# Performance work log

Measured on AMD Instinct MI355X. Metric: run time of the kernel, lower is better.

Reference implementation:

```python
import jax, jax.numpy as jnp
import numpy as np

L, N, E, D_MODEL, H = 3, 50000, 600000, 128, 8
D = D_MODEL // H          # per-head dim = 16
DFF = 4 * D_MODEL         # feedforward hidden = 512


def prelu(x, a):
    return jnp.where(x >= 0, x, a * x)


def layernorm(x, scale, bias, eps=1e-5):
    m = x.mean(-1, keepdims=True)
    v = x.var(-1, keepdims=True)
    return (x - m) * jax.lax.rsqrt(v + eps) * scale + bias


def setup_inputs() -> dict:
    key = jax.random.key(0)
    ks = jax.random.split(key, 16)
    s = 1.0 / np.sqrt(D_MODEL)
    return {
        "in_feats": jax.random.normal(ks[0], (N, D_MODEL), jnp.float32),
        "src": jax.random.randint(ks[1], (E,), 0, N, jnp.int32),
        "dst": jax.random.randint(ks[2], (E,), 0, N, jnp.int32),
        # per-layer stacked parameters
        "W": jax.random.normal(ks[3], (L, D_MODEL, D_MODEL), jnp.float32) * s,
        "attn_l": jax.random.normal(ks[4], (L, H, D), jnp.float32) * s,
        "attn_r": jax.random.normal(ks[5], (L, H, D), jnp.float32) * s,
        "conv_bias": jnp.zeros((L, H, D), jnp.float32),
        "a_conv": jnp.full((L,), 0.25, jnp.float32),   # PReLU slope after conv
        "ln_scale": jnp.ones((L, D_MODEL), jnp.float32),
        "ln_bias": jnp.zeros((L, D_MODEL), jnp.float32),
        "W1": jax.random.normal(ks[6], (L, D_MODEL, DFF), jnp.float32) * s,
        "b1": jnp.zeros((L, DFF), jnp.float32),
        "W2": jax.random.normal(ks[7], (L, DFF, D_MODEL), jnp.float32) / np.sqrt(DFF),
        "b2": jnp.zeros((L, D_MODEL), jnp.float32),
        "a_ff": jnp.full((L,), 0.25, jnp.float32),     # PReLU slope in FF
    }


def _gat_conv(x, src, dst, W, attn_l, attn_r, conv_bias, a_conv):
    # DGL GATConv: project, per-edge additive attention, edge-softmax over dst, scatter.
    z = (x @ W).reshape(N, H, D)                    # [N,H,D]
    el = (z * attn_l).sum(-1)                       # [N,H]
    er = (z * attn_r).sum(-1)                       # [N,H]
    e = jax.nn.leaky_relu(el[src] + er[dst], 0.2)   # [E,H]
    emax = jax.ops.segment_max(e, dst, num_segments=N)
    emax = jnp.where(jnp.isfinite(emax), emax, 0.0)  # zero in-degree guard
    ex = jnp.exp(e - emax[dst])                     # [E,H]
    denom = jax.ops.segment_sum(ex, dst, num_segments=N)  # [N,H]
    msg = ex[:, :, None] * z[src]                   # [E,H,D]
    agg = jax.ops.segment_sum(msg, dst, num_segments=N)   # [N,H,D]
    out = agg / jnp.maximum(denom, 1e-9)[:, :, None]
    out = prelu(out + conv_bias, a_conv)            # bias + PReLU activation
    return out.reshape(N, H * D)


def reference(in_feats, src, dst, W, attn_l, attn_r, conv_bias, a_conv,
              ln_scale, ln_bias, W1, b1, W2, b2, a_ff):
    outputs = []
    x = in_feats
    for l in range(L):
        h = _gat_conv(x, src, dst, W[l], attn_l[l], attn_r[l], conv_bias[l], a_conv[l])
        h = layernorm(h, ln_scale[l], ln_bias[l])   # layer['norm']
        # FeedForward, norm_first=True, sharing the same LayerNorm params
        hn = layernorm(h, ln_scale[l], ln_bias[l])
        ff = prelu(hn @ W1[l] + b1[l], a_ff[l]) @ W2[l] + b2[l]
        x = h + ff
        outputs.append(x)
    return jnp.stack(outputs)                       # [L, N, d]
```

## Files before the change

### kernel.cpp

```cpp
#include <hip/hip_runtime.h>

#define DM 128
#define NH 8
#define DFF 512

typedef __attribute__((ext_vector_type(8))) short bf16x8;
typedef __attribute__((ext_vector_type(4))) float f32x4;

#define WAITVM(N) do { asm volatile("s_waitcnt vmcnt(" #N ")" ::: "memory"); \
                       __builtin_amdgcn_sched_barrier(0); } while (0)
#define WAITLGKM0 do { asm volatile("s_waitcnt lgkmcnt(0)" ::: "memory"); \
                       __builtin_amdgcn_sched_barrier(0); } while (0)

__device__ __forceinline__ short f2bf(float f) {
    union { float f; unsigned u; } v; v.f = f;
    unsigned r = v.u + 0x7fffu + ((v.u >> 16) & 1u);
    return (short)(r >> 16);
}
__device__ __forceinline__ float bf2f(unsigned short b) {
    union { unsigned u; float f; } v; v.u = ((unsigned)b) << 16; return v.f;
}

template<int ROWS, int NT>
__device__ __forceinline__ void stage_tile(
    const short* __restrict__ g, int row0, int maxrow, int rstride, int kbase,
    short* s, int tid)
{
    const int lane = tid & 63;
#pragma unroll
    for (int rr = 0; rr < ROWS * 16 / NT; ++rr) {
        int idx = rr * NT + tid;
        int row = idx >> 4, kc = idx & 15;
        int rg = row0 + row;
        rg = (rg < maxrow) ? rg : (maxrow - 1);
        const short* src = g + (size_t)rg * rstride + kbase
                         + ((kc ^ (row & 15)) << 3);
        short* dst = s + (size_t)(idx - lane) * 8;
        __builtin_amdgcn_global_load_lds(
            (const __attribute__((address_space(1))) void*)src,
            (__attribute__((address_space(3))) void*)dst, 16, 0, 0);
    }
}

__device__ __forceinline__ bf16x8 frag_ld(const short* s, int row, int ks, int g)
{
    return *(const bf16x8*)(s + row * 128 + ((((ks << 2) + g) ^ (row & 15)) << 3));
}

template<bool PRELU, int NOUT>
__global__ __launch_bounds__(512, 4) void gemm_k128_stream(
    const short* __restrict__ A, const short* __restrict__ Bt,
    const float* __restrict__ bias, const float* __restrict__ affp,
    int M, short* __restrict__ outbf)
{
    __shared__ __align__(16) short sW[128 * 128];
    __shared__ __align__(16) short sA[3][64 * 128];

    const int tid = threadIdx.x;
    const int wave = tid >> 6, lane = tid & 63;
    const int wm = wave >> 2, wn = wave & 3;
    const int bn = blockIdx.x * 128;
    const int fr = lane & 15, g = lane >> 4;
    const int lr4 = g << 2;
    const int nT = (M + 63) >> 6;
    const int GY = gridDim.y;
    const int t0 = blockIdx.y;
    const int nLoc = (t0 < nT) ? ((nT - 1 - t0) / GY + 1) : 0;

    float bb[2]; float aff = 0.0f;
    if constexpr (PRELU) {
        aff = *affp;
#pragma unroll
        for (int cg = 0; cg < 2; ++cg)
            bb[cg] = bias[bn + wn * 32 + cg * 16 + fr];
    }

    stage_tile<128, 512>(Bt + (size_t)bn * 128, 0, 128, 128, 0, sW, tid);
    if (nLoc > 0) stage_tile<64, 512>(A, t0 * 64, M, 128, 0, sA[0], tid);
    if (nLoc > 1) stage_tile<64, 512>(A, (t0 + GY) * 64, M, 128, 0, sA[1], tid);

    for (int i = 0; i < nLoc; ++i) {
        const int t = t0 + i * GY;
        if (i >= 1 && i + 1 < nLoc)
            stage_tile<64, 512>(A, (t + GY) * 64, M, 128, 0, sA[(i + 1) % 3], tid);

        if (i == 0) { if (nLoc > 1) { WAITVM(2); } else { WAITVM(0); } }
        else if (i + 1 < nLoc) { WAITVM(18); }
        else { WAITVM(16); }
        __builtin_amdgcn_s_barrier();

        const short* sAb = sA[i % 3];
        f32x4 acc[2][2];
#pragma unroll
        for (int ii = 0; ii < 2; ++ii)
#pragma unroll
            for (int cg = 0; cg < 2; ++cg) acc[ii][cg] = (f32x4)0.0f;

#pragma unroll
        for (int ks = 0; ks < 4; ++ks) {
            bf16x8 af[2], bf[2];
#pragma unroll
            for (int ii = 0; ii < 2; ++ii)
                af[ii] = frag_ld(sAb, wm * 32 + ii * 16 + fr, ks, g);
#pragma unroll
            for (int cg = 0; cg < 2; ++cg)
                bf[cg] = frag_ld(sW, wn * 32 + cg * 16 + fr, ks, g);
#pragma unroll
            for (int ii = 0; ii < 2; ++ii)
#pragma unroll
                for (int cg = 0; cg < 2; ++cg)
                    acc[ii][cg] = __builtin_amdgcn_mfma_f32_16x16x32_bf16(
                        af[ii], bf[cg], acc[ii][cg], 0, 0, 0);
        }

#pragma unroll
        for (int ii = 0; ii < 2; ++ii)
#pragma unroll
            for (int cg = 0; cg < 2; ++cg) {
                int colL = wn * 32 + cg * 16 + fr;
#pragma unroll
                for (int r = 0; r < 4; ++r) {
                    int row = t * 64 + wm * 32 + ii * 16 + lr4 + r;
                    if (row < M) {
                        float v = acc[ii][cg][r];
                        if constexpr (PRELU) {
                            v += bb[cg];
                            v = (v >= 0.0f) ? v : aff * v;
                        }
                        outbf[(size_t)row * NOUT + bn + colL] = f2bf(v);
                    }
                }
            }
    }
}

__global__ __launch_bounds__(512, 2) void ffn2z(
    const short* __restrict__ H1, const short* __restrict__ W2t,
    const short* __restrict__ h_bf, const float* __restrict__ b2,
    const short* __restrict__ Wnt, int has_next, int M,
    float* __restrict__ xo, short* __restrict__ z_next)
{
    __shared__ __align__(16) short sWn[128 * 128];
    __shared__ __align__(16) short sA[2][64 * 128];
    __shared__ __align__(16) short sB[2][128 * 128];

    const int tid = threadIdx.x;
    const int wave = tid >> 6, lane = tid & 63;
    const int wm = wave >> 2, wn = wave & 3;
    const int bm = blockIdx.x * 64;
    const int fr = lane & 15, g = lane >> 4;
    const int lr4 = g << 2;

    f32x4 acc[2][2];
#pragma unroll
    for (int ii = 0; ii < 2; ++ii)
#pragma unroll
        for (int cg = 0; cg < 2; ++cg) acc[ii][cg] = (f32x4)0.0f;

    stage_tile<128, 512>(Wnt, 0, 128, DM, 0, sWn, tid);
    stage_tile<64, 512>(H1, bm, M, DFF, 0, sA[0], tid);
    stage_tile<128, 512>(W2t, 0, 128, DFF, 0, sB[0], tid);

#pragma unroll
    for (int c = 0; c < 4; ++c) {
        __builtin_amdgcn_s_barrier();
        if (c < 3) {
            stage_tile<64, 512>(H1, bm, M, DFF, (c + 1) * 128, sA[(c + 1) & 1], tid);
            stage_tile<128, 512>(W2t, 0, 128, DFF, (c + 1) * 128, sB[(c + 1) & 1], tid);
            WAITVM(6);
        } else {
            WAITVM(0);
        }
        __builtin_amdgcn_s_barrier();

        const short* a = sA[c & 1];
        const short* b = sB[c & 1];
#pragma unroll
        for (int ks = 0; ks < 4; ++ks) {
            bf16x8 af[2], bf[2];
#pragma unroll
            for (int ii = 0; ii < 2; ++ii)
                af[ii] = frag_ld(a, wm * 32 + ii * 16 + fr, ks, g);
#pragma unroll
            for (int cg = 0; cg < 2; ++cg)
                bf[cg] = frag_ld(b, wn * 32 + cg * 16 + fr, ks, g);
#pragma unroll
            for (int ii = 0; ii < 2; ++ii)
#pragma unroll
                for (int cg = 0; cg < 2; ++cg)
                    acc[ii][cg] = __builtin_amdgcn_mfma_f32_16x16x32_bf16(
                        af[ii], bf[cg], acc[ii][cg], 0, 0, 0);
        }
    }

    short* sX = sA[0];
#pragma unroll
    for (int ii = 0; ii < 2; ++ii)
#pragma unroll
        for (int cg = 0; cg < 2; ++cg) {
            int colL = wn * 32 + cg * 16 + fr;
            float bbv = b2[colL];
#pragma unroll
            for (int r = 0; r < 4; ++r) {
                int rowL = wm * 32 + ii * 16 + lr4 + r;
                int row = bm + rowL;
                int rc = (row < M) ? row : (M - 1);
                float v = acc[ii][cg][r] + bbv
                        + bf2f((unsigned short)h_bf[(size_t)rc * DM + colL]);
                if (row < M) xo[(size_t)row * DM + colL] = v;
                if (has_next) {
                    int kc = colL >> 3;
                    sX[rowL * 128 + ((kc ^ (rowL & 15)) << 3) + (colL & 7)]
                        = f2bf(v);
                }
            }
        }
    if (!has_next) return;

    WAITLGKM0;
    __builtin_amdgcn_s_barrier();

    f32x4 acc3[2][2];
#pragma unroll
    for (int ii = 0; ii < 2; ++ii)
#pragma unroll
        for (int cg = 0; cg < 2; ++cg) acc3[ii][cg] = (f32x4)0.0f;

#pragma unroll
    for (int ks = 0; ks < 4; ++ks) {
        bf16x8 af[2], bf[2];
#pragma unroll
        for (int ii = 0; ii < 2; ++ii)
            af[ii] = frag_ld(sX, wm * 32 + ii * 16 + fr, ks, g);
#pragma unroll
        for (int cg = 0; cg < 2; ++cg)
            bf[cg] = frag_ld(sWn, wn * 32 + cg * 16 + fr, ks, g);
#pragma unroll
        for (int ii = 0; ii < 2; ++ii)
#pragma unroll
            for (int cg = 0; cg < 2; ++cg)
                acc3[ii][cg] = __builtin_amdgcn_mfma_f32_16x16x32_bf16(
                    af[ii], bf[cg], acc3[ii][cg], 0, 0, 0);
    }
#pragma unroll
    for (int ii = 0; ii < 2; ++ii)
#pragma unroll
        for (int cg = 0; cg < 2; ++cg) {
            int colL = wn * 32 + cg * 16 + fr;
#pragma unroll
            for (int r = 0; r < 4; ++r) {
                int row = bm + wm * 32 + ii * 16 + lr4 + r;
                if (row < M)
                    z_next[(size_t)row * DM + colL] = f2bf(acc3[ii][cg][r]);
            }
        }
}

__global__ void conv_all_kernel(
    const float* __restrict__ W, const float* __restrict__ W1,
    const float* __restrict__ W2, const float* __restrict__ xin,
    short* __restrict__ Wt, short* __restrict__ W1t, short* __restrict__ W2t,
    short* __restrict__ xbf, int nFeat, int nL)
{
    int idx = blockIdx.x * blockDim.x + threadIdx.x;
    const int n0 = nL * DM * DM, n1 = nL * DM * DFF, n2 = nL * DFF * DM;
    if (idx < n0) {
        int l = idx / (DM * DM), rem = idx & (DM * DM - 1);
        int r = rem >> 7, c = rem & 127;
        Wt[(size_t)l * DM * DM + c * DM + r] = f2bf(W[idx]);
        return;
    }
    idx -= n0;
    if (idx < n1) {
        int l = idx / (DM * DFF), rem = idx & (DM * DFF - 1);
        int r = rem >> 9, c = rem & 511;
        W1t[(size_t)l * DM * DFF + (size_t)c * DM + r] = f2bf(W1[idx]);
        return;
    }
    idx -= n1;
    if (idx < n2) {
        int l = idx / (DFF * DM), rem = idx & (DFF * DM - 1);
        int r = rem >> 7, c = rem & 127;
        W2t[(size_t)l * DFF * DM + (size_t)c * DFF + r] = f2bf(W2[idx]);
        return;
    }
    idx -= n2;
    if (idx < nFeat) xbf[idx] = f2bf(xin[idx]);
}

__global__ void el_er_kernel(const short* __restrict__ z,
                             const float* __restrict__ al,
                             const float* __restrict__ ar,
                             float* __restrict__ el, float* __restrict__ er, int N)
{
    int idx = blockIdx.x * blockDim.x + threadIdx.x;
    if (idx >= N * NH) return;
    int n = idx >> 3, h = idx & 7;
    const unsigned* zp = (const unsigned*)(z + (size_t)n * DM + h * 16);
    const float* alp = al + h * 16;
    const float* arp = ar + h * 16;
    float sl = 0.0f, sr = 0.0f;
#pragma unroll
    for (int d2 = 0; d2 < 8; ++d2) {
        unsigned u = zp[d2];
        float z0 = bf2f((unsigned short)(u & 0xffff));
        float z1 = bf2f((unsigned short)(u >> 16));
        sl = fmaf(z0, alp[2 * d2], sl);     sl = fmaf(z1, alp[2 * d2 + 1], sl);
        sr = fmaf(z0, arp[2 * d2], sr);     sr = fmaf(z1, arp[2 * d2 + 1], sr);
    }
    el[idx] = sl;
    er[idx] = sr;
}

__global__ void hist_kernel(const int* __restrict__ dst, int* __restrict__ deg, int E)
{
    int e = blockIdx.x * blockDim.x + threadIdx.x;
    if (e < E) atomicAdd(&deg[dst[e]], 1);
}

__global__ void scan1_kernel(const int* __restrict__ deg, int* __restrict__ incl,
                             int* __restrict__ bsum, int N)
{
    __shared__ int sm[256];
    int i = blockIdx.x * 256 + threadIdx.x;
    int v = (i < N) ? deg[i] : 0;
    sm[threadIdx.x] = v;
    __syncthreads();
    for (int off = 1; off < 256; off <<= 1) {
        int t = (threadIdx.x >= off) ? sm[threadIdx.x - off] : 0;
        __syncthreads();
        sm[threadIdx.x] += t;
        __syncthreads();
    }
    if (i < N) incl[i] = sm[threadIdx.x];
    if (threadIdx.x == 255) bsum[blockIdx.x] = sm[255];
}

__global__ void scan2_kernel(int* __restrict__ bsum, int nb)
{
    __shared__ int sm[256];
    int v = (threadIdx.x < nb) ? bsum[threadIdx.x] : 0;
    sm[threadIdx.x] = v;
    __syncthreads();
    for (int off = 1; off < 256; off <<= 1) {
        int t = (threadIdx.x >= off) ? sm[threadIdx.x - off] : 0;
        __syncthreads();
        sm[threadIdx.x] += t;
        __syncthreads();
    }
    if (threadIdx.x < nb) bsum[threadIdx.x] = sm[threadIdx.x];
}

__global__ void scan3_kernel(const int* __restrict__ incl, const int* __restrict__ bsum,
                             int* __restrict__ row_ptr, int N)
{
    int i = blockIdx.x * 256 + threadIdx.x;
    if (i < N) {
        int off = (blockIdx.x > 0) ? bsum[blockIdx.x - 1] : 0;
        row_ptr[i + 1] = incl[i] + off;
    }
    if (i == 0) row_ptr[0] = 0;
}

__global__ void scatter_kernel(const int* __restrict__ src, const int* __restrict__ dst,
                               const int* __restrict__ row_ptr, int* __restrict__ cursor,
                               int* __restrict__ csr_src, int E)
{
    int e = blockIdx.x * blockDim.x + threadIdx.x;
    if (e >= E) return;
    int t = dst[e];
    int pos = atomicAdd(&cursor[t], 1);
    csr_src[row_ptr[t] + pos] = src[e];
}

__global__ __launch_bounds__(256) void gat_agg_ln_kernel(
    const int* __restrict__ row_ptr, const int* __restrict__ csr_src,
    const short* __restrict__ z, const float* __restrict__ el,
    const float* __restrict__ er, const float* __restrict__ cb,
    const float* __restrict__ a_conv,
    const float* __restrict__ scale, const float* __restrict__ bias,
    short* __restrict__ h_out, short* __restrict__ hn_out, int N)
{
    int wave = threadIdx.x >> 6, lane = threadIdx.x & 63;
    int t = blockIdx.x * 4 + wave;
    if (t >= N) return;
    int h = lane >> 3;
    int c0 = 2 * lane, c1 = c0 + 1;
    float er_t = er[t * NH + h];
    int e0 = row_ptr[t], e1 = row_ptr[t + 1];
    float acc0 = 0.0f, acc1 = 0.0f, den = 0.0f;
    const unsigned* zw = (const unsigned*)z;

    int e = e0;
    int s[8];
    bool have = (e + 8 <= e1);
    if (have) {
#pragma unroll
        for (int k = 0; k < 8; ++k) s[k] = csr_src[e + k];
    }
    while (have) {
        float x[8]; unsigned u[8];
#pragma unroll
        for (int k = 0; k < 8; ++k) x[k] = el[s[k] * NH + h];
#pragma unroll
        for (int k = 0; k < 8; ++k) u[k] = zw[(size_t)s[k] * 64 + lane];
        int en = e + 8;
        bool hv2 = (en + 8 <= e1);
        int sn[8];
#pragma unroll
        for (int k = 0; k < 8; ++k) sn[k] = hv2 ? csr_src[en + k] : 0;
#pragma unroll
        for (int k = 0; k < 8; ++k) {
            float v = x[k] + er_t;
            v = (v >= 0.0f) ? v : 0.2f * v;
            float w = __expf(v);
            den += w;
            acc0 = fmaf(w, bf2f((unsigned short)(u[k] & 0xffff)), acc0);
            acc1 = fmaf(w, bf2f((unsigned short)(u[k] >> 16)),   acc1);
        }
#pragma unroll
        for (int k = 0; k < 8; ++k) s[k] = sn[k];
        e = en; have = hv2;
    }
    for (; e + 4 <= e1; e += 4) {
        int s4[4];
#pragma unroll
        for (int k = 0; k < 4; ++k) s4[k] = csr_src[e + k];
        float x[4]; unsigned u[4];
#pragma unroll
        for (int k = 0; k < 4; ++k) x[k] = el[s4[k] * NH + h];
#pragma unroll
        for (int k = 0; k < 4; ++k) u[k] = zw[(size_t)s4[k] * 64 + lane];
#pragma unroll
        for (int k = 0; k < 4; ++k) {
            float v = x[k] + er_t;
            v = (v >= 0.0f) ? v : 0.2f * v;
            float w = __expf(v);
            den += w;
            acc0 = fmaf(w, bf2f((unsigned short)(u[k] & 0xffff)), acc0);
            acc1 = fmaf(w, bf2f((unsigned short)(u[k] >> 16)),   acc1);
        }
    }
    for (; e < e1; ++e) {
        int sv = csr_src[e];
        float v = el[sv * NH + h] + er_t;
        v = (v >= 0.0f) ? v : 0.2f * v;
        float w = __expf(v);
        den += w;
        unsigned u = zw[(size_t)sv * 64 + lane];
        acc0 = fmaf(w, bf2f((unsigned short)(u & 0xffff)), acc0);
        acc1 = fmaf(w, bf2f((unsigned short)(u >> 16)), acc1);
    }

    float a = *a_conv;
    float inv = 1.0f / fmaxf(den, 1e-9f);
    float o0 = acc0 * inv + cb[c0];
    float o1 = acc1 * inv + cb[c1];
    o0 = (o0 >= 0.0f) ? o0 : a * o0;
    o1 = (o1 >= 0.0f) ? o1 : a * o1;

    float sc0 = scale[c0], sc1 = scale[c1];
    float bi0 = bias[c0], bi1 = bias[c1];

    float s1 = o0 + o1, ss = o0 * o0 + o1 * o1;
#pragma unroll
    for (int off = 32; off > 0; off >>= 1) {
        s1 += __shfl_xor(s1, off, 64);
        ss += __shfl_xor(ss, off, 64);
    }
    float mean = s1 * (1.0f / 128.0f);
    float var = ss * (1.0f / 128.0f) - mean * mean;
    float rstd = rsqrtf(var + 1e-5f);
    float h0 = (o0 - mean) * rstd * sc0 + bi0;
    float h1 = (o1 - mean) * rstd * sc1 + bi1;
    unsigned hlo = (unsigned short)f2bf(h0);
    unsigned hhi = (unsigned short)f2bf(h1);
    ((unsigned*)h_out)[(size_t)t * 64 + lane] = hlo | (hhi << 16);

    s1 = h0 + h1; ss = h0 * h0 + h1 * h1;
#pragma unroll
    for (int off = 32; off > 0; off >>= 1) {
        s1 += __shfl_xor(s1, off, 64);
        ss += __shfl_xor(ss, off, 64);
    }
    mean = s1 * (1.0f / 128.0f);
    var = ss * (1.0f / 128.0f) - mean * mean;
    rstd = rsqrtf(var + 1e-5f);
    unsigned lo = (unsigned short)f2bf((h0 - mean) * rstd * sc0 + bi0);
    unsigned hi = (unsigned short)f2bf((h1 - mean) * rstd * sc1 + bi1);
    ((unsigned*)hn_out)[(size_t)t * 64 + lane] = lo | (hi << 16);
}

extern "C" void kernel_launch(void* const* d_in, const int* in_sizes, int n_in,
                              void* d_out, int out_size, void* d_ws, size_t ws_size,
                              hipStream_t stream)
{
    const float* in_feats = (const float*)d_in[0];
    const int*   src      = (const int*)d_in[1];
    const int*   dst      = (const int*)d_in[2];
    const float* W        = (const float*)d_in[3];
    const float* attn_l   = (const float*)d_in[4];
    const float* attn_r   = (const float*)d_in[5];
    const float* convb    = (const float*)d_in[6];
    const float* a_conv   = (const float*)d_in[7];
    const float* ln_scale = (const float*)d_in[8];
    const float* ln_bias  = (const float*)d_in[9];
    const float* W1       = (const float*)d_in[10];
    const float* b1       = (const float*)d_in[11];
    const float* W2       = (const float*)d_in[12];
    const float* b2       = (const float*)d_in[13];
    const float* a_ff     = (const float*)d_in[14];
    float* out = (float*)d_out;

    const int N = in_sizes[0] / DM;
    const int E = in_sizes[1];
    const int L = in_sizes[7];

    char* wsb = (char*)d_ws;
    size_t off = 0;
    auto alloc = [&](size_t bytes) { char* p = wsb + off; off += (bytes + 255) & ~(size_t)255; return p; };

    short* z_bf  = (short*)alloc((size_t)N * DM * sizeof(short));
    short* h_bf  = (short*)alloc((size_t)N * DM * sizeof(short));
    short* hn_bf = (short*)alloc((size_t)N * DM * sizeof(short));
    short* x_bf  = (short*)alloc((size_t)N * DM * sizeof(short));
    short* H1    = (short*)alloc((size_t)N * DFF * sizeof(short));
    float* el    = (float*)alloc((size_t)N * NH * sizeof(float));
    float* er    = (float*)alloc((size_t)N * NH * sizeof(float));
    short* Wt    = (short*)alloc((size_t)L * DM * DM * sizeof(short));
    short* W1t   = (short*)alloc((size_t)L * DFF * DM * sizeof(short));
    short* W2t   = (short*)alloc((size_t)L * DM * DFF * sizeof(short));
    int* deg     = (int*)alloc((size_t)N * sizeof(int));
    int* incl    = (int*)alloc((size_t)N * sizeof(int));
    int* bsum    = (int*)alloc(256 * sizeof(int));
    int* row_ptr = (int*)alloc((size_t)(N + 1) * sizeof(int));
    int* cursor  = (int*)alloc((size_t)N * sizeof(int));
    int* csr_src = (int*)alloc((size_t)E * sizeof(int));

    const int gM64  = (N + 63) / 64;
    const int nbScan = (N + 255) / 256;

    hipMemsetAsync(deg, 0, (size_t)N * sizeof(int), stream);
    hipMemsetAsync(cursor, 0, (size_t)N * sizeof(int), stream);
    hist_kernel<<<(E + 255) / 256, 256, 0, stream>>>(dst, deg, E);
    scan1_kernel<<<nbScan, 256, 0, stream>>>(deg, incl, bsum, N);
    scan2_kernel<<<1, 256, 0, stream>>>(bsum, nbScan);
    scan3_kernel<<<nbScan, 256, 0, stream>>>(incl, bsum, row_ptr, N);
    scatter_kernel<<<(E + 255) / 256, 256, 0, stream>>>(src, dst, row_ptr, cursor, csr_src, E);

    {
        int total = L * DM * DM + L * DM * DFF + L * DFF * DM + N * DM;
        conv_all_kernel<<<(total + 255) / 256, 256, 0, stream>>>(
            W, W1, W2, in_feats, Wt, W1t, W2t, x_bf, N * DM, L);
    }

    gemm_k128_stream<false, DM><<<dim3(1, 512), 512, 0, stream>>>(
        x_bf, Wt, nullptr, nullptr, N, z_bf);
    el_er_kernel<<<(N * NH + 255) / 256, 256, 0, stream>>>(
        z_bf, attn_l, attn_r, el, er, N);

    for (int l = 0; l < L; ++l) {
        float* xo = out + (size_t)l * N * DM;
        const int has_next = (l + 1 < L) ? 1 : 0;
        const short* Wnt = has_next ? (Wt + (size_t)(l + 1) * DM * DM) : Wt;

        gat_agg_ln_kernel<<<(N + 3) / 4, 256, 0, stream>>>(
            row_ptr, csr_src, z_bf, el, er, convb + (size_t)l * DM, a_conv + l,
            ln_scale + (size_t)l * DM, ln_bias + (size_t)l * DM, h_bf, hn_bf, N);

        gemm_k128_stream<true, DFF><<<dim3(4, 128), 512, 0, stream>>>(
            hn_bf, W1t + (size_t)l * DFF * DM, b1 + (size_t)l * DFF, a_ff + l, N, H1);

        ffn2z<<<gM64, 512, 0, stream>>>(
            H1, W2t + (size_t)l * DM * DFF, h_bf, b2 + (size_t)l * DM,
            Wnt, has_next, N, xo, z_bf);

        if (has_next)
            el_er_kernel<<<(N * NH + 255) / 256, 256, 0, stream>>>(
                z_bf, attn_l + (size_t)(l + 1) * NH * 16,
                attn_r + (size_t)(l + 1) * NH * 16, el, er, N);
    }
}
```

Measured before the change: 504.0 us.

## Fuse FFN up-projection into FFN2 kernel and halve-wave GAT aggregation

Merges the W1 GEMM (with bias and PReLU) into the FFN2 plus next-layer projection kernel. The 64x512 hidden activation now stays in LDS instead of round-tripping through global memory, and the W1, W2 and Wn weight tiles stream through a shared double buffer. Separately, the GAT aggregation kernel now maps one destination node to half a wave with 4 channels per lane, using 8-byte gathers. The fusion removes a kernel launch and the H1 traffic, at the cost of larger LDS use (sH is 64KB), which may lower occupancy, and a longer serial chain of barriers.

```diff
diff --git a/kernel.cpp b/kernel.cpp
--- a/kernel.cpp
+++ b/kernel.cpp
@@ -6,6 +6,7 @@
 
 typedef __attribute__((ext_vector_type(8))) short bf16x8;
 typedef __attribute__((ext_vector_type(4))) float f32x4;
+typedef __attribute__((ext_vector_type(2))) unsigned uintx2;
 
 #define WAITVM(N) do { asm volatile("s_waitcnt vmcnt(" #N ")" ::: "memory"); \
                        __builtin_amdgcn_sched_barrier(0); } while (0)
@@ -45,6 +46,13 @@
 __device__ __forceinline__ bf16x8 frag_ld(const short* s, int row, int ks, int g)
 {
     return *(const bf16x8*)(s + row * 128 + ((((ks << 2) + g) ^ (row & 15)) << 3));
+}
+
+__device__ __forceinline__ bf16x8 frag_ld_h(const short* s, int row, int c,
+                                            int ks, int g)
+{
+    int ch = ((ks << 2) + g) ^ (row & 15);
+    return *(const bf16x8*)(s + row * 512 + c * 128 + (ch << 3));
 }
 
 template<bool PRELU, int NOUT>
@@ -134,126 +142,172 @@
     }
 }
 
-__global__ __launch_bounds__(512, 2) void ffn2z(
-    const short* __restrict__ H1, const short* __restrict__ W2t,
-    const short* __restrict__ h_bf, const float* __restrict__ b2,
-    const short* __restrict__ Wnt, int has_next, int M,
-    float* __restrict__ xo, short* __restrict__ z_next)
-{
-    __shared__ __align__(16) short sWn[128 * 128];
-    __shared__ __align__(16) short sA[2][64 * 128];
-    __shared__ __align__(16) short sB[2][128 * 128];
+__global__ __launch_bounds__(512, 2) void ffn12z(
+    const short* __restrict__ hn, const short* __restrict__ W1t,
+    const short* __restrict__ W2t, const short* __restrict__ h_bf,
+    const float* __restrict__ b1, const float* __restrict__ b2,
+    const float* __restrict__ affp, const short* __restrict__ Wnt,
+    int has_next, int M, float* __restrict__ xo, short* __restrict__ z_next)
+{
+    __shared__ __align__(16) short sH[64 * 512];
+    __shared__ __align__(16) short sW[2][128 * 128];
 
     const int tid = threadIdx.x;
     const int wave = tid >> 6, lane = tid & 63;
     const int wm = wave >> 2, wn = wave & 3;
     const int bm = blockIdx.x * 64;
     const int fr = lane & 15, g = lane >> 4;
-    const int lr4 = g << 2;
-
-    f32x4 acc[2][2];
+    const int lr4 = g << 2, fk8 = g << 3;
+
+    stage_tile<128, 512>(W1t, 0, 512, 128, 0, sW[0], tid);
+
+    bf16x8 ah[2][4];
+#pragma unroll
+    for (int ii = 0; ii < 2; ++ii) {
+        int row = bm + wm * 32 + ii * 16 + fr;
+        row = (row < M) ? row : (M - 1);
+#pragma unroll
+        for (int ks = 0; ks < 4; ++ks)
+            ah[ii][ks] = *(const bf16x8*)(hn + (size_t)row * DM + ks * 32 + fk8);
+    }
+    float aff = *affp;
+
+    f32x4 acc2[2][2];
 #pragma unroll
     for (int ii = 0; ii < 2; ++ii)
 #pragma unroll
-        for (int cg = 0; cg < 2; ++cg) acc[ii][cg] = (f32x4)0.0f;
-
-    stage_tile<128, 512>(Wnt, 0, 128, DM, 0, sWn, tid);
-    stage_tile<64, 512>(H1, bm, M, DFF, 0, sA[0], tid);
-    stage_tile<128, 512>(W2t, 0, 128, DFF, 0, sB[0], tid);
-
-#pragma unroll
-    for (int c = 0; c < 4; ++c) {
-        __builtin_amdgcn_s_barrier();
-        if (c < 3) {
-            stage_tile<64, 512>(H1, bm, M, DFF, (c + 1) * 128, sA[(c + 1) & 1], tid);
-            stage_tile<128, 512>(W2t, 0, 128, DFF, (c + 1) * 128, sB[(c + 1) & 1], tid);
-            WAITVM(6);
+        for (int cg = 0; cg < 2; ++cg) acc2[ii][cg] = (f32x4)0.0f;
+
+#pragma unroll
+    for (int j = 0; j < 9; ++j) {
+        if (j >= 1) { WAITLGKM0; __builtin_amdgcn_s_barrier(); }
+        if (j + 1 < 9) {
+            int jj = j + 1;
+            if (jj < 4)
+                stage_tile<128, 512>(W1t, jj * 128, 512, 128, 0, sW[jj & 1], tid);
+            else if (jj < 8)
+                stage_tile<128, 512>(W2t, 0, 128, 512, (jj - 4) * 128, sW[jj & 1], tid);
+            else
+                stage_tile<128, 512>(Wnt, 0, 128, 128, 0, sW[jj & 1], tid);
+            WAITVM(4);
         } else {
             WAITVM(0);
         }
         __builtin_amdgcn_s_barrier();
 
-        const short* a = sA[c & 1];
-        const short* b = sB[c & 1];
-#pragma unroll
-        for (int ks = 0; ks < 4; ++ks) {
-            bf16x8 af[2], bf[2];
+        if (j < 4) {
+            f32x4 a1[2][2];
 #pragma unroll
             for (int ii = 0; ii < 2; ++ii)
-                af[ii] = frag_ld(a, wm * 32 + ii * 16 + fr, ks, g);
-#pragma unroll
-            for (int cg = 0; cg < 2; ++cg)
-                bf[cg] = frag_ld(b, wn * 32 + cg * 16 + fr, ks, g);
+#pragma unroll
+                for (int cg = 0; cg < 2; ++cg) a1[ii][cg] = (f32x4)0.0f;
+#pragma unroll
+            for (int ks = 0; ks < 4; ++ks) {
+                bf16x8 bf[2];
+#pragma unroll
+                for (int cg = 0; cg < 2; ++cg)
+                    bf[cg] = frag_ld(sW[j & 1], wn * 32 + cg * 16 + fr, ks, g);
+#pragma unroll
+                for (int ii = 0; ii < 2; ++ii)
+#pragma unroll
+                    for (int cg = 0; cg < 2; ++cg)
+                        a1[ii][cg] = __builtin_amdgcn_mfma_f32_16x16x32_bf16(
+                            ah[ii][ks], bf[cg], a1[ii][cg], 0, 0, 0);
+            }
 #pragma unroll
             for (int ii = 0; ii < 2; ++ii)
 #pragma unroll
+                for (int cg = 0; cg < 2; ++cg) {
+                    int colC = wn * 32 + cg * 16 + fr;
+                    float bb = b1[j * 128 + colC];
+#pragma unroll
+                    for (int r = 0; r < 4; ++r) {
+                        int rowL = wm * 32 + ii * 16 + lr4 + r;
+                        float v = a1[ii][cg][r] + bb;
+                        v = (v >= 0.0f) ? v : aff * v;
+                        int ch = (colC >> 3) ^ (rowL & 15);
+                        sH[rowL * 512 + j * 128 + (ch << 3) + (colC & 7)] = f2bf(v);
+                    }
+                }
+        } else if (j < 8) {
+            int c = j - 4;
+#pragma unroll
+            for (int ks = 0; ks < 4; ++ks) {
+                bf16x8 af[2], bf[2];
+#pragma unroll
+                for (int ii = 0; ii < 2; ++ii)
+                    af[ii] = frag_ld_h(sH, wm * 32 + ii * 16 + fr, c, ks, g);
+#pragma unroll
                 for (int cg = 0; cg < 2; ++cg)
-                    acc[ii][cg] = __builtin_amdgcn_mfma_f32_16x16x32_bf16(
-                        af[ii], bf[cg], acc[ii][cg], 0, 0, 0);
-        }
-    }
-
-    short* sX = sA[0];
-#pragma unroll
-    for (int ii = 0; ii < 2; ++ii)
-#pragma unroll
-        for (int cg = 0; cg < 2; ++cg) {
-            int colL = wn * 32 + cg * 16 + fr;
-            float bbv = b2[colL];
-#pragma unroll
-            for (int r = 0; r < 4; ++r) {
-                int rowL = wm * 32 + ii * 16 + lr4 + r;
-                int row = bm + rowL;
-                int rc = (row < M) ? row : (M - 1);
-                float v = acc[ii][cg][r] + bbv
-                        + bf2f((unsigned short)h_bf[(size_t)rc * DM + colL]);
-                if (row < M) xo[(size_t)row * DM + colL] = v;
-                if (has_next) {
-                    int kc = colL >> 3;
-                    sX[rowL * 128 + ((kc ^ (rowL & 15)) << 3) + (colL & 7)]
-                        = f2bf(v);
+                    bf[cg] = frag_ld(sW[j & 1], wn * 32 + cg * 16 + fr, ks, g);
+#pragma unroll
+                for (int ii = 0; ii < 2; ++ii)
+#pragma unroll
+                    for (int cg = 0; cg < 2; ++cg)
+                        acc2[ii][cg] = __builtin_amdgcn_mfma_f32_16x16x32_bf16(
+                            af[ii], bf[cg], acc2[ii][cg], 0, 0, 0);
+            }
+        } else {
+#pragma unroll
+            for (int ii = 0; ii < 2; ++ii)
+#pragma unroll
+                for (int cg = 0; cg < 2; ++cg) {
+                    int colL = wn * 32 + cg * 16 + fr;
+                    float bbv = b2[colL];
+#pragma unroll
+                    for (int r = 0; r < 4; ++r) {
+                        int rowL = wm * 32 + ii * 16 + lr4 + r;
+                        int row = bm + rowL;
+                        int rc = (row < M) ? row : (M - 1);
+                        float v = acc2[ii][cg][r] + bbv
+                                + bf2f((unsigned short)h_bf[(size_t)rc * DM + colL]);
+                        if (row < M) xo[(size_t)row * DM + colL] = v;
+                        if (has_next) {
+                            int kc = colL >> 3;
+                            sH[rowL * 128 + ((kc ^ (rowL & 15)) << 3) + (colL & 7)]
+                                = f2bf(v);
+                        }
+                    }
                 }
+            if (has_next) {
+                WAITLGKM0;
+                __builtin_amdgcn_s_barrier();
+                f32x4 a3[2][2];
+#pragma unroll
+                for (int ii = 0; ii < 2; ++ii)
+#pragma unroll
+                    for (int cg = 0; cg < 2; ++cg) a3[ii][cg] = (f32x4)0.0f;
+#pragma unroll
+                for (int ks = 0; ks < 4; ++ks) {
+                    bf16x8 af[2], bf[2];
+#pragma unroll
+                    for (int ii = 0; ii < 2; ++ii)
+                        af[ii] = frag_ld(sH, wm * 32 + ii * 16 + fr, ks, g);
+#pragma unroll
+                    for (int cg = 0; cg < 2; ++cg)
+                        bf[cg] = frag_ld(sW[0], wn * 32 + cg * 16 + fr, ks, g);
+#pragma unroll
+                    for (int ii = 0; ii < 2; ++ii)
+#pragma unroll
+                        for (int cg = 0; cg < 2; ++cg)
+                            a3[ii][cg] = __builtin_amdgcn_mfma_f32_16x16x32_bf16(
+                                af[ii], bf[cg], a3[ii][cg], 0, 0, 0);
+                }
+#pragma unroll
+                for (int ii = 0; ii < 2; ++ii)
+#pragma unroll
+                    for (int cg = 0; cg < 2; ++cg) {
+                        int colL = wn * 32 + cg * 16 + fr;
+#pragma unroll
+                        for (int r = 0; r < 4; ++r) {
+                            int row = bm + wm * 32 + ii * 16 + lr4 + r;
+                            if (row < M)
+                                z_next[(size_t)row * DM + colL] = f2bf(a3[ii][cg][r]);
+                        }
+                    }
             }
         }
-    if (!has_next) return;
-
-    WAITLGKM0;
-    __builtin_amdgcn_s_barrier();
-
-    f32x4 acc3[2][2];
-#pragma unroll
-    for (int ii = 0; ii < 2; ++ii)
-#pragma unroll
-        for (int cg = 0; cg < 2; ++cg) acc3[ii][cg] = (f32x4)0.0f;
-
-#pragma unroll
-    for (int ks = 0; ks < 4; ++ks) {
-        bf16x8 af[2], bf[2];
-#pragma unroll
-        for (int ii = 0; ii < 2; ++ii)
-            af[ii] = frag_ld(sX, wm * 32 + ii * 16 + fr, ks, g);
-#pragma unroll
-        for (int cg = 0; cg < 2; ++cg)
-            bf[cg] = frag_ld(sWn, wn * 32 + cg * 16 + fr, ks, g);
-#pragma unroll
-        for (int ii = 0; ii < 2; ++ii)
-#pragma unroll
-            for (int cg = 0; cg < 2; ++cg)
-                acc3[ii][cg] = __builtin_amdgcn_mfma_f32_16x16x32_bf16(
-                    af[ii], bf[cg], acc3[ii][cg], 0, 0, 0);
-    }
-#pragma unroll
-    for (int ii = 0; ii < 2; ++ii)
-#pragma unroll
-        for (int cg = 0; cg < 2; ++cg) {
-            int colL = wn * 32 + cg * 16 + fr;
-#pragma unroll
-            for (int r = 0; r < 4; ++r) {
-                int row = bm + wm * 32 + ii * 16 + lr4 + r;
-                if (row < M)
-                    z_next[(size_t)row * DM + colL] = f2bf(acc3[ii][cg][r]);
-            }
-        }
+    }
 }
 
 __global__ void conv_all_kernel(
@@ -382,14 +436,14 @@
     short* __restrict__ h_out, short* __restrict__ hn_out, int N)
 {
     int wave = threadIdx.x >> 6, lane = threadIdx.x & 63;
-    int t = blockIdx.x * 4 + wave;
+    int half = lane >> 5, l32 = lane & 31;
+    int t = blockIdx.x * 8 + wave * 2 + half;
     if (t >= N) return;
-    int h = lane >> 3;
-    int c0 = 2 * lane, c1 = c0 + 1;
+    int h = l32 >> 2;
+    int cbase = l32 * 4;
     float er_t = er[t * NH + h];
     int e0 = row_ptr[t], e1 = row_ptr[t + 1];
-    float acc0 = 0.0f, acc1 = 0.0f, den = 0.0f;
-    const unsigned* zw = (const unsigned*)z;
+    float a0 = 0.0f, a1 = 0.0f, a2 = 0.0f, a3 = 0.0f, den = 0.0f;
 
     int e = e0;
     int s[8];
@@ -399,11 +453,12 @@
         for (int k = 0; k < 8; ++k) s[k] = csr_src[e + k];
     }
     while (have) {
-        float x[8]; unsigned u[8];
+        float x[8]; uintx2 u[8];
 #pragma unroll
         for (int k = 0; k < 8; ++k) x[k] = el[s[k] * NH + h];
 #pragma unroll
-        for (int k = 0; k < 8; ++k) u[k] = zw[(size_t)s[k] * 64 + lane];
+        for (int k = 0; k < 8; ++k)
+            u[k] = *(const uintx2*)(z + (size_t)s[k] * DM + cbase);
         int en = e + 8;
         bool hv2 = (en + 8 <= e1);
         int sn[8];
@@ -415,8 +470,11 @@
             v = (v >= 0.0f) ? v : 0.2f * v;
             float w = __expf(v);
             den += w;
-            acc0 = fmaf(w, bf2f((unsigned short)(u[k] & 0xffff)), acc0);
-            acc1 = fmaf(w, bf2f((unsigned short)(u[k] >> 16)),   acc1);
+            unsigned w0 = u[k][0], w1 = u[k][1];
+            a0 = fmaf(w, bf2f((unsigned short)(w0 & 0xffff)), a0);
+            a1 = fmaf(w, bf2f((unsigned short)(w0 >> 16)),    a1);
+            a2 = fmaf(w, bf2f((unsigned short)(w1 & 0xffff)), a2);
+            a3 = fmaf(w, bf2f((unsigned short)(w1 >> 16)),    a3);
         }
 #pragma unroll
         for (int k = 0; k < 8; ++k) s[k] = sn[k];
@@ -426,19 +484,23 @@
         int s4[4];
 #pragma unroll
         for (int k = 0; k < 4; ++k) s4[k] = csr_src[e + k];
-        float x[4]; unsigned u[4];
+        float x[4]; uintx2 u[4];
 #pragma unroll
         for (int k = 0; k < 4; ++k) x[k] = el[s4[k] * NH + h];
 #pragma unroll
-        for (int k = 0; k < 4; ++k) u[k] = zw[(size_t)s4[k] * 64 + lane];
+        for (int k = 0; k < 4; ++k)
+            u[k] = *(const uintx2*)(z + (size_t)s4[k] * DM + cbase);
 #pragma unroll
         for (int k = 0; k < 4; ++k) {
             float v = x[k] + er_t;
             v = (v >= 0.0f) ? v : 0.2f * v;
             float w = __expf(v);
             den += w;
-            acc0 = fmaf(w, bf2f((unsigned short)(u[k] & 0xffff)), acc0);
-            acc1 = fmaf(w, bf2f((unsigned short)(u[k] >> 16)),   acc1);
+            unsigned w0 = u[k][0], w1 = u[k][1];
+            a0 = fmaf(w, bf2f((unsigned short)(w0 & 0xffff)), a0);
+            a1 = fmaf(w, bf2f((unsigned short)(w0 >> 16)),    a1);
+            a2 = fmaf(w, bf2f((unsigned short)(w1 & 0xffff)), a2);
+            a3 = fmaf(w, bf2f((unsigned short)(w1 >> 16)),    a3);
         }
     }
     for (; e < e1; ++e) {
@@ -447,48 +509,69 @@
         v = (v >= 0.0f) ? v : 0.2f * v;
         float w = __expf(v);
         den += w;
-        unsigned u = zw[(size_t)sv * 64 + lane];
-        acc0 = fmaf(w, bf2f((unsigned short)(u & 0xffff)), acc0);
-        acc1 = fmaf(w, bf2f((unsigned short)(u >> 16)), acc1);
+        uintx2 u = *(const uintx2*)(z + (size_t)sv * DM + cbase);
+        unsigned w0 = u[0], w1 = u[1];
+        a0 = fmaf(w, bf2f((unsigned short)(w0 & 0xffff)), a0);
+        a1 = fmaf(w, bf2f((unsigned short)(w0 >> 16)),    a1);
+        a2 = fmaf(w, bf2f((unsigned short)(w1 & 0xffff)), a2);
+        a3 = fmaf(w, bf2f((unsigned short)(w1 >> 16)),    a3);
     }
 
     float a = *a_conv;
     float inv = 1.0f / fmaxf(den, 1e-9f);
-    float o0 = acc0 * inv + cb[c0];
-    float o1 = acc1 * inv + cb[c1];
-    o0 = (o0 >= 0.0f) ? o0 : a * o0;
-    o1 = (o1 >= 0.0f) ? o1 : a * o1;
-
-    float sc0 = scale[c0], sc1 = scale[c1];
-    float bi0 = bias[c0], bi1 = bias[c1];
-
-    float s1 = o0 + o1, ss = o0 * o0 + o1 * o1;
-#pragma unroll
-    for (int off = 32; off > 0; off >>= 1) {
+    float o[4] = { a0 * inv + cb[cbase],     a1 * inv + cb[cbase + 1],
+                   a2 * inv + cb[cbase + 2], a3 * inv + cb[cbase + 3] };
+#pragma unroll
+    for (int j = 0; j < 4; ++j) o[j] = (o[j] >= 0.0f) ? o[j] : a * o[j];
+
+    float sc[4], bi[4];
+#pragma unroll
+    for (int j = 0; j < 4; ++j) { sc[j] = scale[cbase + j]; bi[j] = bias[cbase + j]; }
+
+    float s1 = o[0] + o[1] + o[2] + o[3];
+    float ss = o[0]*o[0] + o[1]*o[1] + o[2]*o[2] + o[3]*o[3];
+#pragma unroll
+    for (int off = 16; off > 0; off >>= 1) {
         s1 += __shfl_xor(s1, off, 64);
         ss += __shfl_xor(ss, off, 64);
     }
     float mean = s1 * (1.0f / 128.0f);
     float var = ss * (1.0f / 128.0f) - mean * mean;
     float rstd = rsqrtf(var + 1e-5f);
-    float h0 = (o0 - mean) * rstd * sc0 + bi0;
-    float h1 = (o1 - mean) * rstd * sc1 + bi1;
-    unsigned hlo = (unsigned short)f2bf(h0);
-    unsigned hhi = (unsigned short)f2bf(h1);
-    ((unsigned*)h_out)[(size_t)t * 64 + lane] = hlo | (hhi << 16);
-
-    s1 = h0 + h1; ss = h0 * h0 + h1 * h1;
-#pragma unroll
-    for (int off = 32; off > 0; off >>= 1) {
+    float hv[4];
+#pragma unroll
+    for (int j = 0; j < 4; ++j) hv[j] = (o[j] - mean) * rstd * sc[j] + bi[j];
+    {
+        uintx2 p;
+        p[0] = (unsigned)(unsigned short)f2bf(hv[0])
+             | ((unsigned)(unsigned short)f2bf(hv[1]) << 16);
+        p[1] = (unsigned)(unsigned short)f2bf(hv[2])
+             | ((unsigned)(unsigned short)f2bf(hv[3]) << 16);
+        *(uintx2*)(h_out + (size_t)t * DM + cbase) = p;
+    }
+
+    s1 = hv[0] + hv[1] + hv[2] + hv[3];
+    ss = hv[0]*hv[0] + hv[1]*hv[1] + hv[2]*hv[2] + hv[3]*hv[3];
+#pragma unroll
+    for (int off = 16; off > 0; off >>= 1) {
         s1 += __shfl_xor(s1, off, 64);
         ss += __shfl_xor(ss, off, 64);
     }
     mean = s1 * (1.0f / 128.0f);
     var = ss * (1.0f / 128.0f) - mean * mean;
     rstd = rsqrtf(var + 1e-5f);
-    unsigned lo = (unsigned short)f2bf((h0 - mean) * rstd * sc0 + bi0);
-    unsigned hi = (unsigned short)f2bf((h1 - mean) * rstd * sc1 + bi1);
-    ((unsigned*)hn_out)[(size_t)t * 64 + lane] = lo | (hi << 16);
+    {
+        uintx2 p;
+        float n0 = (hv[0] - mean) * rstd * sc[0] + bi[0];
+        float n1 = (hv[1] - mean) * rstd * sc[1] + bi[1];
+        float n2 = (hv[2] - mean) * rstd * sc[2] + bi[2];
+        float n3 = (hv[3] - mean) * rstd * sc[3] + bi[3];
+        p[0] = (unsigned)(unsigned short)f2bf(n0)
+             | ((unsigned)(unsigned short)f2bf(n1) << 16);
+        p[1] = (unsigned)(unsigned short)f2bf(n2)
+             | ((unsigned)(unsigned short)f2bf(n3) << 16);
+        *(uintx2*)(hn_out + (size_t)t * DM + cbase) = p;
+    }
 }
 
 extern "C" void kernel_launch(void* const* d_in, const int* in_sizes, int n_in,
@@ -524,7 +607,6 @@
     short* h_bf  = (short*)alloc((size_t)N * DM * sizeof(short));
     short* hn_bf = (short*)alloc((size_t)N * DM * sizeof(short));
     short* x_bf  = (short*)alloc((size_t)N * DM * sizeof(short));
-    short* H1    = (short*)alloc((size_t)N * DFF * sizeof(short));
     float* el    = (float*)alloc((size_t)N * NH * sizeof(float));
     float* er    = (float*)alloc((size_t)N * NH * sizeof(float));
     short* Wt    = (short*)alloc((size_t)L * DM * DM * sizeof(short));
@@ -564,15 +646,13 @@
         const int has_next = (l + 1 < L) ? 1 : 0;
         const short* Wnt = has_next ? (Wt + (size_t)(l + 1) * DM * DM) : Wt;
 
-        gat_agg_ln_kernel<<<(N + 3) / 4, 256, 0, stream>>>(
+        gat_agg_ln_kernel<<<(N + 7) / 8, 256, 0, stream>>>(
             row_ptr, csr_src, z_bf, el, er, convb + (size_t)l * DM, a_conv + l,
             ln_scale + (size_t)l * DM, ln_bias + (size_t)l * DM, h_bf, hn_bf, N);
 
-        gemm_k128_stream<true, DFF><<<dim3(4, 128), 512, 0, stream>>>(
-            hn_bf, W1t + (size_t)l * DFF * DM, b1 + (size_t)l * DFF, a_ff + l, N, H1);
-
-        ffn2z<<<gM64, 512, 0, stream>>>(
-            H1, W2t + (size_t)l * DM * DFF, h_bf, b2 + (size_t)l * DM,
+        ffn12z<<<gM64, 512, 0, stream>>>(
+            hn_bf, W1t + (size_t)l * DFF * DM, W2t + (size_t)l * DM * DFF,
+            h_bf, b1 + (size_t)l * DFF, b2 + (size_t)l * DM, a_ff + l,
             Wnt, has_next, N, xo, z_bf);
 
         if (has_next)
```

New measurement: 498.2 us. Within noise of the previous version (-1.1%).
